# Optimization experiments

Measured on AMD Instinct MI355X. Metric: run time of the kernel, lower is better.

Reference implementation:

```python
import jax, jax.numpy as jnp
import numpy as np

NUM_HEADS = 8
NEG_INF = -1e9

def setup_inputs() -> dict:
    key = jax.random.key(0)
    k1, k2 = jax.random.split(key)
    B, S, D = 2, 4096, 512
    inputs = jax.random.normal(k1, (B, S, D), dtype=jnp.float32)
    # glorot-style scale for the fused QKV weight
    qkv_weights = jax.random.normal(k2, (D, 3 * D), dtype=jnp.float32) * (1.0 / np.sqrt(D))
    return {"inputs": inputs, "qkv_weights": qkv_weights}

def reference(inputs, qkv_weights):
    B, S, D = inputs.shape
    H = NUM_HEADS
    d = D // H  # head dim
    qkv = jnp.einsum('bsd,de->bse', inputs, qkv_weights)  # (B,S,3D)
    q, k, v = jnp.split(qkv, 3, axis=-1)
    # (B,S,D) -> (B,H,S,d)
    def split_heads(x):
        return x.reshape(B, S, H, d).transpose(0, 2, 1, 3)
    q, k, v = split_heads(q), split_heads(k), split_heads(v)
    scores = jnp.einsum('bhid,bhjd->bhij', q, k) / jnp.sqrt(jnp.asarray(d, inputs.dtype))
    # causal mask as in source: tril * scores + (-1e9) * upper-triangle
    tril = jnp.tril(jnp.ones((S, S), dtype=inputs.dtype))
    scores = tril * scores + NEG_INF * (1.0 - tril)
    a = jax.nn.softmax(scores, axis=-1)
    out = jnp.einsum('bhij,bhjd->bhid', a, v)  # (B,H,S,d)
    return out.transpose(0, 2, 1, 3).reshape(B, S, D)
```

## Files before the change

kernel.cpp:

```cpp
#include <hip/hip_runtime.h>

typedef unsigned short u16;
typedef __bf16 b16;
typedef b16 b16x8 __attribute__((ext_vector_type(8)));
typedef float f32x4 __attribute__((ext_vector_type(4)));
typedef u16 u16x4 __attribute__((ext_vector_type(4)));
typedef u16 u16x8 __attribute__((ext_vector_type(8)));
typedef float f4 __attribute__((ext_vector_type(4)));

#define NH 8
#define SEQ 4096
#define DM 512
#define HDIM 64
#define GM 8192
#define GK 512
#define GN 1536

#define QSCALE 0.18033688011112042f
#define SMBIAS 14.0f

__device__ __forceinline__ u16 f2bf(float f) {
  b16 h = (b16)f;
  return __builtin_bit_cast(u16, h);
}

__device__ __forceinline__ void gl16(const u16* g, u16* l) {
  __builtin_amdgcn_global_load_lds((const __attribute__((address_space(1))) void*)g,
                                   (__attribute__((address_space(3))) void*)l, 16, 0, 0);
}

__global__ __launch_bounds__(256) void cvt_inputs(const float* __restrict__ x,
                                                  u16* __restrict__ y) {
  int i = (blockIdx.x * 256 + threadIdx.x) * 8;
  f4 a = *(const f4*)(x + i);
  f4 b = *(const f4*)(x + i + 4);
  u16x8 o;
  o[0] = f2bf(a[0]); o[1] = f2bf(a[1]); o[2] = f2bf(a[2]); o[3] = f2bf(a[3]);
  o[4] = f2bf(b[0]); o[5] = f2bf(b[1]); o[6] = f2bf(b[2]); o[7] = f2bf(b[3]);
  *(u16x8*)(y + i) = o;
}

__global__ __launch_bounds__(256) void cvt_w(const float* __restrict__ w,
                                             u16* __restrict__ wt) {
  __shared__ float tile[32][33];
  int n0 = blockIdx.x * 32;
  int k0 = blockIdx.y * 32;
  int t = threadIdx.x;
  int tn = t & 31, tk = t >> 5;
#pragma unroll
  for (int p = 0; p < 4; ++p) {
    int k = tk + p * 8;
    tile[k][tn] = w[(k0 + k) * GN + n0 + tn];
  }
  __syncthreads();
  int n_l = t >> 3, kg = (t & 7) * 4;
  u16x4 o;
#pragma unroll
  for (int i = 0; i < 4; ++i) o[i] = f2bf(tile[kg + i][n_l]);
  *(u16x4*)(wt + (n0 + n_l) * GK + k0 + kg) = o;
}

__global__ __launch_bounds__(256, 3) void qkv_gemm(const u16* __restrict__ A,
                                                   const u16* __restrict__ Wt,
                                                   u16* __restrict__ Q,
                                                   u16* __restrict__ K,
                                                   u16* __restrict__ V) {
  __shared__ __align__(16) u16 As[3][4096];
  __shared__ __align__(16) u16 Bs[3][4096];
  int bm = blockIdx.x * 128;
  int bn = blockIdx.y * 128;
  int t = threadIdx.x;
  int lane = t & 63, w = t >> 6;
  int wr = w >> 1, wc = w & 1;
  int l15 = lane & 15, g = lane >> 4;

  f32x4 acc[4][4];
#pragma unroll
  for (int i = 0; i < 4; ++i)
#pragma unroll
    for (int j = 0; j < 4; ++j) {
      acc[i][j][0] = 0.f; acc[i][j][1] = 0.f; acc[i][j][2] = 0.f; acc[i][j][3] = 0.f;
    }

#define GSTAGE(slot, k0) do {                                                   \
    _Pragma("unroll")                                                           \
    for (int p = 0; p < 2; ++p) {                                               \
      int cid = p * 256 + t;                                                    \
      int row = cid >> 2, co = (cid & 3) * 8;                                   \
      gl16(A + (size_t)(bm + row) * GK + (k0) + co, &As[slot][cid * 8]);        \
      gl16(Wt + (size_t)(bn + row) * GK + (k0) + co, &Bs[slot][cid * 8]);       \
    }                                                                           \
  } while (0)

  GSTAGE(0, 0);
  GSTAGE(1, 32);
  int cur = 0;
  for (int kk = 0; kk < 16; ++kk) {
    asm volatile("s_waitcnt vmcnt(4)" ::: "memory");
    __builtin_amdgcn_s_barrier();
    int pk = kk + 2 < 16 ? kk + 2 : 15;
    int slot = cur + 2; if (slot >= 3) slot -= 3;
    GSTAGE(slot, pk * 32);

    b16x8 af[4], bf[4];
#pragma unroll
    for (int mi = 0; mi < 4; ++mi)
      af[mi] = *(const b16x8*)(&As[cur][(wr * 64 + mi * 16 + l15) * 32 + g * 8]);
#pragma unroll
    for (int ni = 0; ni < 4; ++ni)
      bf[ni] = *(const b16x8*)(&Bs[cur][(wc * 64 + ni * 16 + l15) * 32 + g * 8]);
    __builtin_amdgcn_s_setprio(1);
#pragma unroll
    for (int mi = 0; mi < 4; ++mi)
#pragma unroll
      for (int ni = 0; ni < 4; ++ni)
        acc[mi][ni] = __builtin_amdgcn_mfma_f32_16x16x32_bf16(af[mi], bf[ni], acc[mi][ni], 0, 0, 0);
    __builtin_amdgcn_s_setprio(0);
    cur = (cur == 2) ? 0 : cur + 1;
  }

#pragma unroll
  for (int mi = 0; mi < 4; ++mi)
#pragma unroll
    for (int ni = 0; ni < 4; ++ni) {
      int e = bn + wc * 64 + ni * 16 + l15;
      int which = e >> 9, col = e & 511;
      int h = col >> 6, dd = col & 63;
      u16* dst = which == 0 ? Q : (which == 1 ? K : V);
      float scale = (which == 0) ? QSCALE : 1.0f;
#pragma unroll
      for (int r = 0; r < 4; ++r) {
        int m = bm + wr * 64 + mi * 16 + g * 4 + r;
        int b = m >> 12, s = m & 4095;
        dst[(((b * NH + h) * SEQ) + s) * HDIM + dd] = f2bf(acc[mi][ni][r] * scale);
      }
    }
}

__global__ __launch_bounds__(256) void transpose_v(const u16* __restrict__ V,
                                                   u16* __restrict__ Vt) {
  __shared__ u16 tl[64][72];
  int bh = blockIdx.x >> 6;
  int s0 = (blockIdx.x & 63) * 64;
  const u16* src = V + ((size_t)bh * SEQ + s0) * HDIM;
  u16* dst = Vt + (size_t)bh * HDIM * SEQ + s0;
  int t = threadIdx.x;
#pragma unroll
  for (int p = 0; p < 2; ++p) {
    int cid = p * 256 + t;
    int row = cid >> 3, ch = cid & 7;
    *(u16x8*)(&tl[row][ch * 8]) = *(const u16x8*)(src + row * HDIM + ch * 8);
  }
  __syncthreads();
#pragma unroll
  for (int p = 0; p < 4; ++p) {
    int cid = p * 256 + t;
    int dd = cid >> 4, l = cid & 15;
    u16x4 o;
#pragma unroll
    for (int c = 0; c < 4; ++c) o[c] = tl[c * 16 + l][dd];
    *(u16x4*)(dst + dd * SEQ + l * 4) = o;
  }
}

__global__ __launch_bounds__(256, 4) void attn(const u16* __restrict__ Q,
                                               const u16* __restrict__ Kv,
                                               const u16* __restrict__ Vtg,
                                               float* __restrict__ out) {
  int id = blockIdx.x;
  int bh = id & 15;
  int qt = 63 - (id >> 4);
  int b = bh >> 3, h = bh & 7;
  const u16* Qb = Q + (size_t)bh * SEQ * HDIM;
  const u16* Kb = Kv + (size_t)bh * SEQ * HDIM;
  const u16* Vb = Vtg + (size_t)bh * HDIM * SEQ;
  int t = threadIdx.x, lane = t & 63, w = t >> 6;
  int l15 = lane & 15, g = lane >> 4;
  int qb = qt * 64;
  int qw = qb + w * 16;

  __shared__ __align__(16) u16 Ks[2][4096];
  __shared__ __align__(16) u16 Vs[2][4096];
  __shared__ __align__(16) u16 Ps[4096];

  int rsub = lane >> 3, cp = lane & 7;
  int ch = cp ^ rsub;
  int xorp = (l15 & 7) << 3;

  b16x8 qf[2];
#pragma unroll
  for (int ks = 0; ks < 2; ++ks)
    qf[ks] = *(const b16x8*)(Qb + (qw + l15) * HDIM + ks * 32 + g * 8);

  b16x8 vone;
#pragma unroll
  for (int i = 0; i < 8; ++i) vone[i] = __builtin_bit_cast(b16, (u16)0x3F80);

  f32x4 oacc[4], lacc;
#pragma unroll
  for (int i = 0; i < 4; ++i) {
    oacc[i][0] = 0.f; oacc[i][1] = 0.f; oacc[i][2] = 0.f; oacc[i][3] = 0.f;
    lacc[i] = 0.f;
  }

#define STAGE(slot, jj) do {                                                    \
    _Pragma("unroll")                                                           \
    for (int p = 0; p < 2; ++p) {                                               \
      int row = (w * 2 + p) * 8 + rsub;                                         \
      gl16(Kb + (size_t)((jj) + row) * HDIM + ch * 8, &Ks[slot][(w * 2 + p) * 512]); \
      gl16(Vb + (size_t)row * SEQ + (jj) + ch * 8, &Vs[slot][(w * 2 + p) * 512]);    \
    }                                                                           \
  } while (0)

#define QKT(sx, slot) do {                                                      \
    _Pragma("unroll")                                                           \
    for (int c = 0; c < 4; ++c) {                                               \
      sx[c][0] = -SMBIAS; sx[c][1] = -SMBIAS; sx[c][2] = -SMBIAS; sx[c][3] = -SMBIAS; \
    }                                                                           \
    _Pragma("unroll")                                                           \
    for (int c = 0; c < 4; ++c) {                                               \
      const u16* kr = Ks[slot] + (c * 16 + l15) * 64;                           \
      b16x8 kf0 = *(const b16x8*)(kr + ((g * 8) ^ xorp));                       \
      b16x8 kf1 = *(const b16x8*)(kr + ((32 + g * 8) ^ xorp));                  \
      sx[c] = __builtin_amdgcn_mfma_f32_16x16x32_bf16(qf[0], kf0, sx[c], 0, 0, 0); \
      sx[c] = __builtin_amdgcn_mfma_f32_16x16x32_bf16(qf[1], kf1, sx[c], 0, 0, 0); \
    }                                                                           \
  } while (0)

#define SMSTORE(sx, jj) do {                                                    \
    if ((jj) + 63 > qw) {                                                       \
      _Pragma("unroll")                                                         \
      for (int c = 0; c < 4; ++c)                                               \
        _Pragma("unroll")                                                       \
        for (int r = 0; r < 4; ++r) {                                           \
          int col = (jj) + c * 16 + l15;                                        \
          int qq = qw + g * 4 + r;                                              \
          if (col > qq) sx[c][r] = -1e30f;                                      \
        }                                                                       \
    }                                                                           \
    _Pragma("unroll")                                                           \
    for (int r = 0; r < 4; ++r) {                                               \
      u16x4 pw;                                                                 \
      _Pragma("unroll")                                                         \
      for (int c = 0; c < 4; ++c)                                               \
        pw[c] = f2bf(__builtin_amdgcn_exp2f(sx[c][r]));                         \
      int prow = w * 16 + g * 4 + r;                                            \
      *(u16x4*)(Ps + prow * 64 + ((l15 * 4) ^ ((prow & 7) << 3))) = pw;         \
    }                                                                           \
  } while (0)

  int nt = qt + 1;

  STAGE(0, 0);
  asm volatile("s_waitcnt vmcnt(0)" ::: "memory");
  __builtin_amdgcn_s_barrier();
  if (nt > 1) STAGE(1, 64);
  {
    f32x4 s0[4];
    QKT(s0, 0);
    SMSTORE(s0, 0);
  }

  int cur = 0;
  for (int tt = 0; tt < nt; ++tt) {
    asm volatile("s_waitcnt vmcnt(0)" ::: "memory");
    __builtin_amdgcn_s_barrier();

    b16x8 vfr[2][4];
#pragma unroll
    for (int js = 0; js < 2; ++js)
#pragma unroll
      for (int tdd = 0; tdd < 4; ++tdd)
        vfr[js][tdd] = *(const b16x8*)(Vs[cur] + (tdd * 16 + l15) * 64 + ((js * 32 + g * 8) ^ xorp));
    asm volatile("s_waitcnt lgkmcnt(0)" ::: "memory");
    __builtin_amdgcn_s_barrier();

    if (tt + 2 < nt) STAGE(cur, (tt + 2) * 64);

    bool more = (tt + 1 < nt);
    f32x4 sb[4];
    __builtin_amdgcn_s_setprio(1);
    if (more) QKT(sb, cur ^ 1);

#pragma unroll
    for (int js = 0; js < 2; ++js) {
      int eoff = (js * 32 + g * 8) ^ xorp;
      b16x8 pf = *(const b16x8*)(Ps + (w * 16 + l15) * 64 + eoff);
      lacc = __builtin_amdgcn_mfma_f32_16x16x32_bf16(pf, vone, lacc, 0, 0, 0);
#pragma unroll
      for (int tdd = 0; tdd < 4; ++tdd)
        oacc[tdd] = __builtin_amdgcn_mfma_f32_16x16x32_bf16(pf, vfr[js][tdd], oacc[tdd], 0, 0, 0);
    }
    __builtin_amdgcn_s_setprio(0);

    if (more) SMSTORE(sb, (tt + 1) * 64);
    cur ^= 1;
  }

  float inv[4];
#pragma unroll
  for (int r = 0; r < 4; ++r) inv[r] = 1.0f / lacc[r];
#pragma unroll
  for (int tdd = 0; tdd < 4; ++tdd)
#pragma unroll
    for (int r = 0; r < 4; ++r) {
      int q = qw + g * 4 + r;
      int dd = tdd * 16 + l15;
      out[((size_t)b * SEQ + q) * DM + h * HDIM + dd] = oacc[tdd][r] * inv[r];
    }
}

extern "C" void kernel_launch(void* const* d_in, const int* in_sizes, int n_in,
                              void* d_out, int out_size, void* d_ws, size_t ws_size,
                              hipStream_t stream) {
  const float* x = (const float*)d_in[0];
  const float* wq = (const float*)d_in[1];
  float* out = (float*)d_out;
  char* ws = (char*)d_ws;

  u16* A  = (u16*)ws;
  u16* Wt = (u16*)(ws + 8388608);
  u16* Qw = (u16*)(ws + 8388608 + 1572864);
  u16* Kw = Qw + 4194304;
  u16* Vw = Kw + 4194304;
  u16* Vt = A;

  cvt_inputs<<<2048, 256, 0, stream>>>(x, A);
  dim3 gw(48, 16);
  cvt_w<<<gw, 256, 0, stream>>>(wq, Wt);
  dim3 gg(64, 12);
  qkv_gemm<<<gg, 256, 0, stream>>>(A, Wt, Qw, Kw, Vw);
  transpose_v<<<1024, 256, 0, stream>>>(Vw, Vt);
  attn<<<1024, 256, 0, stream>>>(Qw, Kw, Vt, out);
}
```

Baseline: 99.34 us.

## Split long causal attention tiles across KV halves and fuse V transpose into GEMM

Query tiles in the upper half now have their KV range split across two blocks, writing unnormalized partial outputs and row sums that a new normalize kernel combines and divides. The standalone V transpose kernel is removed by having the QKV GEMM epilogue write V directly in transposed layout, and the two fp32-to-bf16 conversion kernels are merged into one launch. This is meant to even out causal load imbalance and cut launches and memory passes. It adds an extra normalize pass over the output, and the strided Vt stores in the GEMM epilogue may be poorly coalesced.

Result: slower. 113.2 us (+13.9%).

```diff
diff --git a/kernel.cpp b/kernel.cpp
--- a/kernel.cpp
+++ b/kernel.cpp
@@ -29,42 +29,45 @@
                                    (__attribute__((address_space(3))) void*)l, 16, 0, 0);
 }
 
-__global__ __launch_bounds__(256) void cvt_inputs(const float* __restrict__ x,
-                                                  u16* __restrict__ y) {
-  int i = (blockIdx.x * 256 + threadIdx.x) * 8;
-  f4 a = *(const f4*)(x + i);
-  f4 b = *(const f4*)(x + i + 4);
-  u16x8 o;
-  o[0] = f2bf(a[0]); o[1] = f2bf(a[1]); o[2] = f2bf(a[2]); o[3] = f2bf(a[3]);
-  o[4] = f2bf(b[0]); o[5] = f2bf(b[1]); o[6] = f2bf(b[2]); o[7] = f2bf(b[3]);
-  *(u16x8*)(y + i) = o;
-}
-
-__global__ __launch_bounds__(256) void cvt_w(const float* __restrict__ w,
-                                             u16* __restrict__ wt) {
+__global__ __launch_bounds__(256) void cvt_fused(const float* __restrict__ x,
+                                                 u16* __restrict__ y,
+                                                 const float* __restrict__ w,
+                                                 u16* __restrict__ wt) {
   __shared__ float tile[32][33];
-  int n0 = blockIdx.x * 32;
-  int k0 = blockIdx.y * 32;
+  int bid = blockIdx.x;
   int t = threadIdx.x;
-  int tn = t & 31, tk = t >> 5;
-#pragma unroll
-  for (int p = 0; p < 4; ++p) {
-    int k = tk + p * 8;
-    tile[k][tn] = w[(k0 + k) * GN + n0 + tn];
-  }
-  __syncthreads();
-  int n_l = t >> 3, kg = (t & 7) * 4;
-  u16x4 o;
-#pragma unroll
-  for (int i = 0; i < 4; ++i) o[i] = f2bf(tile[kg + i][n_l]);
-  *(u16x4*)(wt + (n0 + n_l) * GK + k0 + kg) = o;
+  if (bid < 2048) {
+    int i = (bid * 256 + t) * 8;
+    f4 a = *(const f4*)(x + i);
+    f4 b = *(const f4*)(x + i + 4);
+    u16x8 o;
+    o[0] = f2bf(a[0]); o[1] = f2bf(a[1]); o[2] = f2bf(a[2]); o[3] = f2bf(a[3]);
+    o[4] = f2bf(b[0]); o[5] = f2bf(b[1]); o[6] = f2bf(b[2]); o[7] = f2bf(b[3]);
+    *(u16x8*)(y + i) = o;
+  } else {
+    int q = bid - 2048;
+    int n0 = (q % 48) * 32;
+    int k0 = (q / 48) * 32;
+    int tn = t & 31, tk = t >> 5;
+#pragma unroll
+    for (int p = 0; p < 4; ++p) {
+      int k = tk + p * 8;
+      tile[k][tn] = w[(k0 + k) * GN + n0 + tn];
+    }
+    __syncthreads();
+    int n_l = t >> 3, kg = (t & 7) * 4;
+    u16x4 o;
+#pragma unroll
+    for (int i2 = 0; i2 < 4; ++i2) o[i2] = f2bf(tile[kg + i2][n_l]);
+    *(u16x4*)(wt + (n0 + n_l) * GK + k0 + kg) = o;
+  }
 }
 
 __global__ __launch_bounds__(256, 3) void qkv_gemm(const u16* __restrict__ A,
                                                    const u16* __restrict__ Wt,
                                                    u16* __restrict__ Q,
                                                    u16* __restrict__ K,
-                                                   u16* __restrict__ V) {
+                                                   u16* __restrict__ Vt) {
   __shared__ __align__(16) u16 As[3][4096];
   __shared__ __align__(16) u16 Bs[3][4096];
   int bm = blockIdx.x * 128;
@@ -126,50 +129,43 @@
       int e = bn + wc * 64 + ni * 16 + l15;
       int which = e >> 9, col = e & 511;
       int h = col >> 6, dd = col & 63;
-      u16* dst = which == 0 ? Q : (which == 1 ? K : V);
-      float scale = (which == 0) ? QSCALE : 1.0f;
-#pragma unroll
-      for (int r = 0; r < 4; ++r) {
-        int m = bm + wr * 64 + mi * 16 + g * 4 + r;
-        int b = m >> 12, s = m & 4095;
-        dst[(((b * NH + h) * SEQ) + s) * HDIM + dd] = f2bf(acc[mi][ni][r] * scale);
+      if (which < 2) {
+        u16* dst = which == 0 ? Q : K;
+        float scale = (which == 0) ? QSCALE : 1.0f;
+#pragma unroll
+        for (int r = 0; r < 4; ++r) {
+          int m = bm + wr * 64 + mi * 16 + g * 4 + r;
+          int b = m >> 12, s = m & 4095;
+          dst[(((b * NH + h) * SEQ) + s) * HDIM + dd] = f2bf(acc[mi][ni][r] * scale);
+        }
+      } else {
+#pragma unroll
+        for (int r = 0; r < 4; ++r) {
+          int m = bm + wr * 64 + mi * 16 + g * 4 + r;
+          int b = m >> 12, s = m & 4095;
+          int sp = (s & ~63) | ((g * 4 + r) * 4 + mi);
+          Vt[((size_t)(b * NH + h) * HDIM + dd) * SEQ + sp] = f2bf(acc[mi][ni][r]);
+        }
       }
     }
-}
-
-__global__ __launch_bounds__(256) void transpose_v(const u16* __restrict__ V,
-                                                   u16* __restrict__ Vt) {
-  __shared__ u16 tl[64][72];
-  int bh = blockIdx.x >> 6;
-  int s0 = (blockIdx.x & 63) * 64;
-  const u16* src = V + ((size_t)bh * SEQ + s0) * HDIM;
-  u16* dst = Vt + (size_t)bh * HDIM * SEQ + s0;
-  int t = threadIdx.x;
-#pragma unroll
-  for (int p = 0; p < 2; ++p) {
-    int cid = p * 256 + t;
-    int row = cid >> 3, ch = cid & 7;
-    *(u16x8*)(&tl[row][ch * 8]) = *(const u16x8*)(src + row * HDIM + ch * 8);
-  }
-  __syncthreads();
-#pragma unroll
-  for (int p = 0; p < 4; ++p) {
-    int cid = p * 256 + t;
-    int dd = cid >> 4, l = cid & 15;
-    u16x4 o;
-#pragma unroll
-    for (int c = 0; c < 4; ++c) o[c] = tl[c * 16 + l][dd];
-    *(u16x4*)(dst + dd * SEQ + l * 4) = o;
-  }
 }
 
 __global__ __launch_bounds__(256, 4) void attn(const u16* __restrict__ Q,
                                                const u16* __restrict__ Kv,
                                                const u16* __restrict__ Vtg,
-                                               float* __restrict__ out) {
+                                               float* __restrict__ out,
+                                               float* __restrict__ Opart,
+                                               float* __restrict__ l0,
+                                               float* __restrict__ l1) {
   int id = blockIdx.x;
   int bh = id & 15;
-  int qt = 63 - (id >> 4);
+  int i = id >> 4;
+  int qt, ts; bool primary;
+  if (i < 32)      { qt = 32 + i; ts = 0;  primary = true;  }
+  else if (i < 64) { qt = 95 - i; ts = 32; primary = false; }
+  else             { qt = i - 64; ts = 0;  primary = true;  }
+  int te = (i < 32) ? 31 : qt;
+
   int b = bh >> 3, h = bh & 7;
   const u16* Qb = Q + (size_t)bh * SEQ * HDIM;
   const u16* Kb = Kv + (size_t)bh * SEQ * HDIM;
@@ -194,13 +190,13 @@
 
   b16x8 vone;
 #pragma unroll
-  for (int i = 0; i < 8; ++i) vone[i] = __builtin_bit_cast(b16, (u16)0x3F80);
+  for (int ii = 0; ii < 8; ++ii) vone[ii] = __builtin_bit_cast(b16, (u16)0x3F80);
 
   f32x4 oacc[4], lacc;
 #pragma unroll
-  for (int i = 0; i < 4; ++i) {
-    oacc[i][0] = 0.f; oacc[i][1] = 0.f; oacc[i][2] = 0.f; oacc[i][3] = 0.f;
-    lacc[i] = 0.f;
+  for (int ii = 0; ii < 4; ++ii) {
+    oacc[ii][0] = 0.f; oacc[ii][1] = 0.f; oacc[ii][2] = 0.f; oacc[ii][3] = 0.f;
+    lacc[ii] = 0.f;
   }
 
 #define STAGE(slot, jj) do {                                                    \
@@ -249,20 +245,20 @@
     }                                                                           \
   } while (0)
 
-  int nt = qt + 1;
-
-  STAGE(0, 0);
+  int nt = te - ts + 1;
+
+  STAGE(0, ts * 64);
   asm volatile("s_waitcnt vmcnt(0)" ::: "memory");
   __builtin_amdgcn_s_barrier();
-  if (nt > 1) STAGE(1, 64);
+  if (nt > 1) STAGE(1, (ts + 1) * 64);
   {
     f32x4 s0[4];
     QKT(s0, 0);
-    SMSTORE(s0, 0);
+    SMSTORE(s0, ts * 64);
   }
 
   int cur = 0;
-  for (int tt = 0; tt < nt; ++tt) {
+  for (int tt = ts; tt <= te; ++tt) {
     asm volatile("s_waitcnt vmcnt(0)" ::: "memory");
     __builtin_amdgcn_s_barrier();
 
@@ -275,9 +271,9 @@
     asm volatile("s_waitcnt lgkmcnt(0)" ::: "memory");
     __builtin_amdgcn_s_barrier();
 
-    if (tt + 2 < nt) STAGE(cur, (tt + 2) * 64);
-
-    bool more = (tt + 1 < nt);
+    if (tt + 2 <= te) STAGE(cur, (tt + 2) * 64);
+
+    bool more = (tt < te);
     f32x4 sb[4];
     __builtin_amdgcn_s_setprio(1);
     if (more) QKT(sb, cur ^ 1);
@@ -297,17 +293,57 @@
     cur ^= 1;
   }
 
-  float inv[4];
-#pragma unroll
-  for (int r = 0; r < 4; ++r) inv[r] = 1.0f / lacc[r];
-#pragma unroll
-  for (int tdd = 0; tdd < 4; ++tdd)
-#pragma unroll
-    for (int r = 0; r < 4; ++r) {
-      int q = qw + g * 4 + r;
-      int dd = tdd * 16 + l15;
-      out[((size_t)b * SEQ + q) * DM + h * HDIM + dd] = oacc[tdd][r] * inv[r];
-    }
+  if (primary) {
+    if (l15 == 0) {
+#pragma unroll
+      for (int r = 0; r < 4; ++r) l0[bh * SEQ + qw + g * 4 + r] = lacc[r];
+    }
+#pragma unroll
+    for (int tdd = 0; tdd < 4; ++tdd)
+#pragma unroll
+      for (int r = 0; r < 4; ++r) {
+        int q = qw + g * 4 + r;
+        out[((size_t)b * SEQ + q) * DM + h * HDIM + tdd * 16 + l15] = oacc[tdd][r];
+      }
+  } else {
+    if (l15 == 0) {
+#pragma unroll
+      for (int r = 0; r < 4; ++r) l1[bh * SEQ + qw + g * 4 + r] = lacc[r];
+    }
+    float* op = Opart + (size_t)(bh * 32 + (qt - 32)) * 4096;
+#pragma unroll
+    for (int tdd = 0; tdd < 4; ++tdd)
+#pragma unroll
+      for (int r = 0; r < 4; ++r)
+        op[(w * 16 + g * 4 + r) * 64 + tdd * 16 + l15] = oacc[tdd][r];
+  }
+}
+
+__global__ __launch_bounds__(256) void normalize(float* __restrict__ out,
+                                                 const float* __restrict__ Opart,
+                                                 const float* __restrict__ l0,
+                                                 const float* __restrict__ l1) {
+  size_t idx = ((size_t)blockIdx.x * 256 + threadIdx.x) * 8;
+  int dall = (int)(idx & 511);
+  int s = (int)((idx >> 9) & 4095);
+  int b = (int)(idx >> 21);
+  int h = dall >> 6, dd = dall & 63;
+  int bh = b * NH + h;
+  int qt = s >> 6;
+  float l = l0[bh * SEQ + s];
+  f4 v0 = *(f4*)(out + idx);
+  f4 v1 = *(f4*)(out + idx + 4);
+  if (qt >= 32) {
+    l += l1[bh * SEQ + s];
+    const float* op = Opart + (size_t)(bh * 32 + (qt - 32)) * 4096 + (s & 63) * 64 + dd;
+    f4 p0 = *(const f4*)op;
+    f4 p1 = *(const f4*)(op + 4);
+    v0 += p0; v1 += p1;
+  }
+  float inv = 1.0f / l;
+  v0 *= inv; v1 *= inv;
+  *(f4*)(out + idx) = v0;
+  *(f4*)(out + idx + 4) = v1;
 }
 
 extern "C" void kernel_launch(void* const* d_in, const int* in_sizes, int n_in,
@@ -320,16 +356,16 @@
 
   u16* A  = (u16*)ws;
   u16* Wt = (u16*)(ws + 8388608);
-  u16* Qw = (u16*)(ws + 8388608 + 1572864);
+  u16* Qw = (u16*)(ws + 9961472);
   u16* Kw = Qw + 4194304;
-  u16* Vw = Kw + 4194304;
-  u16* Vt = A;
-
-  cvt_inputs<<<2048, 256, 0, stream>>>(x, A);
-  dim3 gw(48, 16);
-  cvt_w<<<gw, 256, 0, stream>>>(wq, Wt);
+  u16* Vt = Kw + 4194304;
+  float* Opart = (float*)ws;
+  float* l0 = (float*)(ws + 8388608);
+  float* l1 = (float*)(ws + 8650752);
+
+  cvt_fused<<<2816, 256, 0, stream>>>(x, A, wq, Wt);
   dim3 gg(64, 12);
-  qkv_gemm<<<gg, 256, 0, stream>>>(A, Wt, Qw, Kw, Vw);
-  transpose_v<<<1024, 256, 0, stream>>>(Vw, Vt);
-  attn<<<1024, 256, 0, stream>>>(Qw, Kw, Vt, out);
-}
+  qkv_gemm<<<gg, 256, 0, stream>>>(A, Wt, Qw, Kw, Vt);
+  attn<<<1536, 256, 0, stream>>>(Qw, Kw, Vt, out, Opart, l0, l1);
+  normalize<<<2048, 256, 0, stream>>>(out, Opart, l0, l1);
+}
```
